# Kernel optimization log

Measured on AMD Instinct MI355X. Metric: run time of the kernel, lower is better.

Reference implementation:

```python
import jax, jax.numpy as jnp
import numpy as np

DIM = 1024

def setup_inputs() -> dict:
    key = jax.random.key(0)
    k1, k2, k3, k4 = jax.random.split(key, 4)
    scale = 1.0 / np.sqrt(DIM)
    return {
        "segment_embeds": jax.random.normal(k1, (32, 2048, DIM), dtype=jnp.float32),
        "Wq": jax.random.normal(k2, (DIM, DIM), dtype=jnp.float32) * scale,
        "bq": jax.random.normal(k3, (DIM,), dtype=jnp.float32) * scale,
        "mem_bank": jax.random.normal(k4, (131072, DIM), dtype=jnp.float32) * scale,
        "k": 8,
    }

def reference(segment_embeds, Wq, bq, mem_bank, k):
    # mean-pool over time: (B, C)
    segment_mean = segment_embeds.mean(axis=1)
    # linear query projection (torch Linear: x @ W.T + b)
    q = segment_mean @ Wq.T + bq
    # dense scores against memory bank: (B, M)
    attn_scores = (q @ mem_bank.T) / jnp.sqrt(jnp.asarray(DIM, dtype=q.dtype))
    # top-k select
    top_k_scores, top_k_indices = jax.lax.top_k(attn_scores, k)  # (B, K)
    attn_weights = jax.nn.softmax(top_k_scores, axis=-1)  # (B, K)
    # gather retrieved vectors: (B, K, C)
    retrieved_vectors = mem_bank[top_k_indices]
    # weighted sum over K, keepdim -> (B, 1, C)
    retrieved_mem = jnp.sum(attn_weights[..., None] * retrieved_vectors, axis=1, keepdims=True)
    return retrieved_mem
```

## Files before the change

### kernel.cpp

```cpp
#include <hip/hip_runtime.h>
#include <hip/hip_bf16.h>
#include <math.h>

#define NB 32
#define NT 2048
#define NC 1024
#define NM 131072
#define TOPK 8
#define NSB 256
#define ROWS_PB 512
#define NP 32
#define SLOTF 260
#define TILEF (4 * 16 * SLOTF)
#define SCOFF (2 * TILEF)
#define SMEMF (SCOFF + 2 * 32 * 17)

typedef __attribute__((ext_vector_type(8))) short s16x8;
typedef __attribute__((ext_vector_type(4))) float f32x4;
typedef __attribute__((ext_vector_type(4))) int i32x4;

#define OFF_PART 0
#define OFF_CS   0
#define OFF_CI   65536
#define OFF_MEAN 1048576
#define OFF_Q    (OFF_MEAN + 32768)
#define OFF_QB   (OFF_Q + 32768)

__device__ __forceinline__ unsigned short f2bf(float f) {
    unsigned u = __float_as_uint(f);
    unsigned r = (u + 0x7FFFu + ((u >> 16) & 1u)) >> 16;
    return (unsigned short)r;
}

__device__ __forceinline__ void gl_lds16(const float* g, float* l) {
    __builtin_amdgcn_global_load_lds((const __attribute__((address_space(1))) void*)g,
                                     (__attribute__((address_space(3))) void*)l, 16, 0, 0);
}

__global__ __launch_bounds__(256) void mean_partial_k(const float* __restrict__ seg,
                                                      float* __restrict__ part) {
    int blk = blockIdx.x;
    int b = blk >> 5, tc = blk & 31;
    int tid = threadIdx.x;
    const float4* src = (const float4*)(seg + ((size_t)b * NT + (size_t)tc * 64) * NC);
    float4 acc = make_float4(0.f, 0.f, 0.f, 0.f);
#pragma unroll 4
    for (int t = 0; t < 64; ++t) {
        float4 v = src[(size_t)t * 256 + tid];
        acc.x += v.x; acc.y += v.y; acc.z += v.z; acc.w += v.w;
    }
    ((float4*)(part + ((size_t)b * 32 + tc) * NC))[tid] = acc;
}

__global__ __launch_bounds__(256) void mean_finalize_k(const float* __restrict__ part,
                                                       float* __restrict__ mean) {
    int i = blockIdx.x * 256 + threadIdx.x;
    int b = i >> 10, c = i & 1023;
    float s = 0.f;
#pragma unroll
    for (int tc = 0; tc < 32; ++tc) s += part[((size_t)b * 32 + tc) * NC + c];
    mean[i] = s * (1.0f / NT);
}

__global__ __launch_bounds__(256) void qproj_k(const float* __restrict__ mean,
                                               const float* __restrict__ Wq,
                                               const float* __restrict__ bq,
                                               float* __restrict__ q) {
    int wave = (blockIdx.x * 256 + threadIdx.x) >> 6;
    int lane = threadIdx.x & 63;
    int o0 = wave * 16;
    for (int j = 0; j < 16; ++j) {
        int o = o0 + j;
        int b = o >> 10, i = o & 1023;
        const float4* wr = (const float4*)(Wq + (size_t)i * NC);
        const float4* mr = (const float4*)(mean + (size_t)b * NC);
        float acc = 0.f;
#pragma unroll
        for (int e = 0; e < 4; ++e) {
            float4 w4 = wr[lane * 4 + e];
            float4 m4 = mr[lane * 4 + e];
            acc += w4.x * m4.x + w4.y * m4.y + w4.z * m4.z + w4.w * m4.w;
        }
#pragma unroll
        for (int off = 32; off; off >>= 1) acc += __shfl_xor(acc, off);
        if (lane == 0) q[o] = acc + bq[i];
    }
}

__global__ __launch_bounds__(256) void qbf_k(const float* __restrict__ q,
                                             s16x8* __restrict__ qb) {
    int idx = blockIdx.x * 256 + threadIdx.x;
    int lane = idx & 63, n = (idx >> 6) & 1, ks = idx >> 7;
    int b = n * 16 + (lane & 15);
    int k0 = ks * 32 + ((lane >> 4) << 3);
    s16x8 v;
#pragma unroll
    for (int e = 0; e < 8; ++e) v[e] = (short)f2bf(q[(size_t)b * NC + k0 + e]);
    qb[idx] = v;
}

#define BUBBLE8(v, vi, s, si)                                   \
    {                                                           \
        float _v = (v); int _vi = (vi);                         \
        _Pragma("unroll")                                       \
        for (int _u = 0; _u < 8; ++_u) {                        \
            bool _gt = _v > s[_u];                               \
            float _ts = _gt ? _v : s[_u];                       \
            int _ti = _gt ? _vi : si[_u];                       \
            _v = _gt ? s[_u] : _v;                              \
            _vi = _gt ? si[_u] : _vi;                           \
            s[_u] = _ts; si[_u] = _ti;                          \
        }                                                       \
    }

#define BUBBLE8F(v, s)                                          \
    {                                                           \
        float _v = (v);                                         \
        _Pragma("unroll")                                       \
        for (int _u = 0; _u < 8; ++_u) {                        \
            bool _gt = _v > s[_u];                               \
            float _ts = _gt ? _v : s[_u];                       \
            _v = _gt ? s[_u] : _v;                              \
            s[_u] = _ts;                                        \
        }                                                       \
    }

__global__ __launch_bounds__(256, 1) void scores_mfma_k(const float* __restrict__ memb,
                                                        const s16x8* __restrict__ qb,
                                                        float* __restrict__ candS,
                                                        int* __restrict__ candI) {
    extern __shared__ __align__(16) float smemf[];
    int tid = threadIdx.x, lane = tid & 63, ws = tid >> 6;
    int n = ws & 1, kh = ws >> 1;
    size_t mb0 = (size_t)blockIdx.x * ROWS_PB;

    float s8[8];
#pragma unroll
    for (int u = 0; u < 8; ++u) s8[u] = -INFINITY;

#define TISSUE(p_) { float* lb = smemf + ((p_) & 1) * TILEF;                          \
    const float* gb = memb + (mb0 + (size_t)(p_) * 16) * NC + lane * 4;               \
    _Pragma("unroll") for (int i_ = 0; i_ < 16; ++i_) {                               \
        int r_ = ws * 4 + (i_ >> 2), c_ = i_ & 3;                                     \
        gl_lds16(gb + (size_t)r_ * NC + c_ * 256, lb + (c_ * 16 + r_) * SLOTF); } }

    s16x8 qf[16];
#pragma unroll
    for (int s = 0; s < 16; ++s)
        qf[s] = qb[((kh * 16 + s) * 2 + n) * 64 + lane];

    TISSUE(0);
    TISSUE(1);

    for (int p = 0; p < NP; ++p) {
        if (p + 1 < NP) { asm volatile("s_waitcnt vmcnt(16)" ::: "memory"); }
        else            { asm volatile("s_waitcnt vmcnt(0)" ::: "memory"); }
        __builtin_amdgcn_sched_barrier(0);
        __builtin_amdgcn_s_barrier();
        __builtin_amdgcn_sched_barrier(0);

        f32x4 acc = (f32x4){0.f, 0.f, 0.f, 0.f};
        const float* tb = smemf + (p & 1) * TILEF;
#pragma unroll
        for (int s = 0; s < 16; ++s) {
            int ksg = kh * 16 + s;
            const float* ap = tb + ((ksg >> 3) * 16 + (lane & 15)) * SLOTF
                            + (ksg & 7) * 32 + ((lane >> 4) << 3);
            uint4 lo = *(const uint4*)(ap);
            uint4 hi = *(const uint4*)(ap + 4);
            i32x4 ai;
            ai[0] = __builtin_amdgcn_perm(lo.y, lo.x, 0x07060302u);
            ai[1] = __builtin_amdgcn_perm(lo.w, lo.z, 0x07060302u);
            ai[2] = __builtin_amdgcn_perm(hi.y, hi.x, 0x07060302u);
            ai[3] = __builtin_amdgcn_perm(hi.w, hi.z, 0x07060302u);
            s16x8 a = __builtin_bit_cast(s16x8, ai);
            acc = __builtin_amdgcn_mfma_f32_16x16x32_bf16(a, qf[s], acc, 0, 0, 0);
        }

        {
            int bcol = n * 16 + (lane & 15);
            int mrow = (lane >> 4) << 2;
#pragma unroll
            for (int j = 0; j < 4; ++j)
                smemf[SCOFF + (kh * 32 + bcol) * 17 + mrow + j] = acc[j];
        }
        asm volatile("s_waitcnt lgkmcnt(0)" ::: "memory");
        __builtin_amdgcn_sched_barrier(0);
        __builtin_amdgcn_s_barrier();
        __builtin_amdgcn_sched_barrier(0);

        {
            int b = tid >> 3, pq = tid & 7;
#pragma unroll
            for (int rr = 0; rr < 2; ++rr) {
                int m = pq + rr * 8;
                float v = smemf[SCOFF + b * 17 + m]
                        + smemf[SCOFF + (32 + b) * 17 + m];
                unsigned uu = (__float_as_uint(v) & ~0x1FFu) | (unsigned)(p * 16 + m);
                BUBBLE8F(__uint_as_float(uu), s8);
            }
        }
        __builtin_amdgcn_sched_barrier(0);
        __builtin_amdgcn_s_barrier();
        __builtin_amdgcn_sched_barrier(0);

        if (p + 2 < NP) TISSUE(p + 2);
    }
#undef TISSUE

    {
        float* cs = smemf;
#pragma unroll
        for (int u = 0; u < 8; ++u) cs[tid * 9 + u] = s8[u];
        __syncthreads();
        float* csA = smemf + 2304;
        if (tid < 64) {
            float s2[8];
#pragma unroll
            for (int u = 0; u < 8; ++u) s2[u] = -INFINITY;
            int t0 = (tid >> 1) * 8 + (tid & 1) * 4;
            for (int tt = 0; tt < 4; ++tt)
#pragma unroll
                for (int u = 0; u < 8; ++u)
                    BUBBLE8F(cs[(t0 + tt) * 9 + u], s2);
#pragma unroll
            for (int u = 0; u < 8; ++u) csA[tid * 9 + u] = s2[u];
        }
        __syncthreads();
        if (tid < 32) {
            float s3[8];
#pragma unroll
            for (int u = 0; u < 8; ++u) s3[u] = -INFINITY;
            for (int j = 0; j < 16; ++j)
                BUBBLE8F(csA[(tid * 2 + (j >> 3)) * 9 + (j & 7)], s3);
#pragma unroll
            for (int u = 0; u < 8; ++u) {
                candS[((size_t)tid * NSB + blockIdx.x) * 8 + u] = s3[u] * 0.03125f;
                candI[((size_t)tid * NSB + blockIdx.x) * 8 + u] =
                    (int)mb0 + (int)(__float_as_uint(s3[u]) & 0x1FFu);
            }
        }
    }
}

__global__ __launch_bounds__(256) void finalize_k(const float* __restrict__ candS,
                                                  const int* __restrict__ candI,
                                                  const float* __restrict__ memb,
                                                  const float* __restrict__ q,
                                                  float* __restrict__ out) {
    __shared__ float cs[256 * 9];
    __shared__ int ci[256 * 9];
    __shared__ float csA[64 * 9];
    __shared__ int ciA[64 * 9];
    __shared__ float exsc[64];
    __shared__ int exid[64];
    __shared__ float wgt[8];
    __shared__ int widx[8];
    int b = blockIdx.x, tid = threadIdx.x;
    const float* S = candS + (size_t)b * (NSB * 8);
    const int* I = candI + (size_t)b * (NSB * 8);

    {
        float s[8]; int si[8];
#pragma unroll
        for (int u = 0; u < 8; ++u) { s[u] = -INFINITY; si[u] = -1; }
        for (int j = 0; j < 8; ++j)
            BUBBLE8(S[tid * 8 + j], I[tid * 8 + j], s, si);
#pragma unroll
        for (int u = 0; u < 8; ++u) { cs[tid * 9 + u] = s[u]; ci[tid * 9 + u] = si[u]; }
    }
    __syncthreads();
    if (tid < 64) {
        float s[8]; int si[8];
#pragma unroll
        for (int u = 0; u < 8; ++u) { s[u] = -INFINITY; si[u] = -1; }
        for (int tt = 0; tt < 4; ++tt)
#pragma unroll
            for (int u = 0; u < 8; ++u)
                BUBBLE8(cs[(tid * 4 + tt) * 9 + u], ci[(tid * 4 + tt) * 9 + u], s, si);
#pragma unroll
        for (int u = 0; u < 8; ++u) { csA[tid * 9 + u] = s[u]; ciA[tid * 9 + u] = si[u]; }
    }
    __syncthreads();
    if (tid < 8) {
        float s[8]; int si[8];
#pragma unroll
        for (int u = 0; u < 8; ++u) { s[u] = -INFINITY; si[u] = -1; }
        for (int tt = 0; tt < 8; ++tt)
#pragma unroll
            for (int u = 0; u < 8; ++u)
                BUBBLE8(csA[(tid * 8 + tt) * 9 + u], ciA[(tid * 8 + tt) * 9 + u], s, si);
#pragma unroll
        for (int u = 0; u < 8; ++u) exid[tid * 8 + u] = si[u];
    }
    __syncthreads();
    {
        int w = tid >> 6, lane = tid & 63;
        const float4* qr = (const float4*)(q + (size_t)b * NC);
        for (int i = 0; i < 16; ++i) {
            int c = w * 16 + i;
            int row = exid[c];
            const float4* mr = (const float4*)(memb + (size_t)row * NC);
            float d = 0.f;
#pragma unroll
            for (int e = 0; e < 4; ++e) {
                float4 m4 = mr[e * 64 + lane];
                float4 q4 = qr[e * 64 + lane];
                d += m4.x * q4.x + m4.y * q4.y + m4.z * q4.z + m4.w * q4.w;
            }
#pragma unroll
            for (int off = 32; off; off >>= 1) d += __shfl_xor(d, off);
            if (lane == 0) exsc[c] = d * 0.03125f;
        }
    }
    __syncthreads();
    if (tid == 0) {
        float s4[8]; int si4[8];
#pragma unroll
        for (int u = 0; u < 8; ++u) { s4[u] = -INFINITY; si4[u] = -1; }
        for (int j = 0; j < 64; ++j)
            BUBBLE8(exsc[j], exid[j], s4, si4);
        float m = s4[0], sum = 0.f, w[8];
#pragma unroll
        for (int u = 0; u < 8; ++u) { w[u] = __expf(s4[u] - m); sum += w[u]; }
        float inv = 1.0f / sum;
#pragma unroll
        for (int u = 0; u < 8; ++u) { wgt[u] = w[u] * inv; widx[u] = si4[u]; }
    }
    __syncthreads();
    {
        float wv[8]; int ix[8];
#pragma unroll
        for (int u = 0; u < 8; ++u) { wv[u] = wgt[u]; ix[u] = widx[u]; }
        float4 o = make_float4(0.f, 0.f, 0.f, 0.f);
#pragma unroll
        for (int u = 0; u < 8; ++u) {
            float4 r = ((const float4*)(memb + (size_t)ix[u] * NC))[tid];
            o.x = fmaf(wv[u], r.x, o.x);
            o.y = fmaf(wv[u], r.y, o.y);
            o.z = fmaf(wv[u], r.z, o.z);
            o.w = fmaf(wv[u], r.w, o.w);
        }
        ((float4*)(out + (size_t)b * NC))[tid] = o;
    }
}

extern "C" void kernel_launch(void* const* d_in, const int* in_sizes, int n_in,
                              void* d_out, int out_size, void* d_ws, size_t ws_size,
                              hipStream_t stream) {
    const float* seg  = (const float*)d_in[0];
    const float* Wq   = (const float*)d_in[1];
    const float* bq   = (const float*)d_in[2];
    const float* memb = (const float*)d_in[3];
    float* ws = (float*)d_ws;
    float* part  = ws + OFF_PART;
    float* mean  = ws + OFF_MEAN;
    float* q     = ws + OFF_Q;
    s16x8* qb    = (s16x8*)(ws + OFF_QB);
    float* candS = ws + OFF_CS;
    int*   candI = (int*)(ws + OFF_CI);
    float* out = (float*)d_out;

    (void)hipFuncSetAttribute((const void*)scores_mfma_k,
                              hipFuncAttributeMaxDynamicSharedMemorySize,
                              SMEMF * 4);

    mean_partial_k<<<NB * 32, 256, 0, stream>>>(seg, part);
    mean_finalize_k<<<(NB * NC) / 256, 256, 0, stream>>>(part, mean);
    qproj_k<<<512, 256, 0, stream>>>(mean, Wq, bq, q);
    qbf_k<<<16, 256, 0, stream>>>(q, qb);
    scores_mfma_k<<<NSB, 256, SMEMF * 4, stream>>>(memb, qb, candS, candI);
    finalize_k<<<NB, 256, 0, stream>>>(candS, candI, memb, q, out);
}
```

Baseline: 204.6 us.

## Double the score-kernel block to 512 threads and stage tiles through registers

Raises the scores kernel to 512 threads (8 waves), splitting the K dimension four ways so each wave runs 8 MFMAs per panel instead of 16. Tiles are now loaded through registers and written to LDS (register double-buffering) instead of the async global_load_lds path, and the per-panel top-k update uses one candidate per thread. The aim is more memory parallelism and latency hiding for streaming the memory bank, at the cost of an extra LDS write pass, more __syncthreads per panel, and a 4-way partial-sum reduction.

```diff
diff --git a/kernel.cpp b/kernel.cpp
--- a/kernel.cpp
+++ b/kernel.cpp
@@ -13,7 +13,7 @@
 #define SLOTF 260
 #define TILEF (4 * 16 * SLOTF)
 #define SCOFF (2 * TILEF)
-#define SMEMF (SCOFF + 2 * 32 * 17)
+#define SMEMF (SCOFF + 4 * 32 * 17)
 
 typedef __attribute__((ext_vector_type(8))) short s16x8;
 typedef __attribute__((ext_vector_type(4))) float f32x4;
@@ -30,11 +30,6 @@
     unsigned u = __float_as_uint(f);
     unsigned r = (u + 0x7FFFu + ((u >> 16) & 1u)) >> 16;
     return (unsigned short)r;
-}
-
-__device__ __forceinline__ void gl_lds16(const float* g, float* l) {
-    __builtin_amdgcn_global_load_lds((const __attribute__((address_space(1))) void*)g,
-                                     (__attribute__((address_space(3))) void*)l, 16, 0, 0);
 }
 
 __global__ __launch_bounds__(256) void mean_partial_k(const float* __restrict__ seg,
@@ -125,7 +120,7 @@
         }                                                       \
     }
 
-__global__ __launch_bounds__(256, 1) void scores_mfma_k(const float* __restrict__ memb,
+__global__ __launch_bounds__(512, 1) void scores_mfma_k(const float* __restrict__ memb,
                                                         const s16x8* __restrict__ qb,
                                                         float* __restrict__ candS,
                                                         int* __restrict__ candI) {
@@ -133,92 +128,92 @@
     int tid = threadIdx.x, lane = tid & 63, ws = tid >> 6;
     int n = ws & 1, kh = ws >> 1;
     size_t mb0 = (size_t)blockIdx.x * ROWS_PB;
+    const float4* gbase = (const float4*)(memb + mb0 * NC);
 
     float s8[8];
 #pragma unroll
     for (int u = 0; u < 8; ++u) s8[u] = -INFINITY;
 
-#define TISSUE(p_) { float* lb = smemf + ((p_) & 1) * TILEF;                          \
-    const float* gb = memb + (mb0 + (size_t)(p_) * 16) * NC + lane * 4;               \
-    _Pragma("unroll") for (int i_ = 0; i_ < 16; ++i_) {                               \
-        int r_ = ws * 4 + (i_ >> 2), c_ = i_ & 3;                                     \
-        gl_lds16(gb + (size_t)r_ * NC + c_ * 256, lb + (c_ * 16 + r_) * SLOTF); } }
-
-    s16x8 qf[16];
-#pragma unroll
-    for (int s = 0; s < 16; ++s)
-        qf[s] = qb[((kh * 16 + s) * 2 + n) * 64 + lane];
-
-    TISSUE(0);
-    TISSUE(1);
-
-    for (int p = 0; p < NP; ++p) {
-        if (p + 1 < NP) { asm volatile("s_waitcnt vmcnt(16)" ::: "memory"); }
-        else            { asm volatile("s_waitcnt vmcnt(0)" ::: "memory"); }
-        __builtin_amdgcn_sched_barrier(0);
-        __builtin_amdgcn_s_barrier();
-        __builtin_amdgcn_sched_barrier(0);
-
-        f32x4 acc = (f32x4){0.f, 0.f, 0.f, 0.f};
-        const float* tb = smemf + (p & 1) * TILEF;
-#pragma unroll
-        for (int s = 0; s < 16; ++s) {
-            int ksg = kh * 16 + s;
-            const float* ap = tb + ((ksg >> 3) * 16 + (lane & 15)) * SLOTF
-                            + (ksg & 7) * 32 + ((lane >> 4) << 3);
-            uint4 lo = *(const uint4*)(ap);
-            uint4 hi = *(const uint4*)(ap + 4);
-            i32x4 ai;
-            ai[0] = __builtin_amdgcn_perm(lo.y, lo.x, 0x07060302u);
-            ai[1] = __builtin_amdgcn_perm(lo.w, lo.z, 0x07060302u);
-            ai[2] = __builtin_amdgcn_perm(hi.y, hi.x, 0x07060302u);
-            ai[3] = __builtin_amdgcn_perm(hi.w, hi.z, 0x07060302u);
-            s16x8 a = __builtin_bit_cast(s16x8, ai);
-            acc = __builtin_amdgcn_mfma_f32_16x16x32_bf16(a, qf[s], acc, 0, 0, 0);
-        }
-
-        {
-            int bcol = n * 16 + (lane & 15);
-            int mrow = (lane >> 4) << 2;
-#pragma unroll
-            for (int j = 0; j < 4; ++j)
-                smemf[SCOFF + (kh * 32 + bcol) * 17 + mrow + j] = acc[j];
-        }
-        asm volatile("s_waitcnt lgkmcnt(0)" ::: "memory");
-        __builtin_amdgcn_sched_barrier(0);
-        __builtin_amdgcn_s_barrier();
-        __builtin_amdgcn_sched_barrier(0);
-
-        {
-            int b = tid >> 3, pq = tid & 7;
-#pragma unroll
-            for (int rr = 0; rr < 2; ++rr) {
-                int m = pq + rr * 8;
-                float v = smemf[SCOFF + b * 17 + m]
-                        + smemf[SCOFF + (32 + b) * 17 + m];
-                unsigned uu = (__float_as_uint(v) & ~0x1FFu) | (unsigned)(p * 16 + m);
-                BUBBLE8F(__uint_as_float(uu), s8);
-            }
-        }
-        __builtin_amdgcn_sched_barrier(0);
-        __builtin_amdgcn_s_barrier();
-        __builtin_amdgcn_sched_barrier(0);
-
-        if (p + 2 < NP) TISSUE(p + 2);
-    }
-#undef TISSUE
+    s16x8 qf[8];
+#pragma unroll
+    for (int s = 0; s < 8; ++s)
+        qf[s] = qb[(((kh * 8 + s) * 2) + n) * 64 + lane];
+
+    int lwoff[8];
+#pragma unroll
+    for (int i = 0; i < 8; ++i) {
+        int f = i * 512 + tid;
+        lwoff[i] = (((f >> 6) & 3) * 16 + (f >> 8)) * SLOTF + (f & 63) * 4;
+    }
+
+#define LOADR(dst_, p_) { const float4* gp = gbase + (size_t)(p_) * 4096;             \
+    _Pragma("unroll") for (int i_ = 0; i_ < 8; ++i_)                                  \
+        dst_[i_] = gp[i_ * 512 + tid];                                                \
+    __builtin_amdgcn_sched_barrier(0); }
+
+#define WRITEL(src_, buf_) { float* lb = smemf + (buf_) * TILEF;                      \
+    _Pragma("unroll") for (int i_ = 0; i_ < 8; ++i_)                                  \
+        *(float4*)(lb + lwoff[i_]) = src_[i_]; }
+
+#define DOPANEL(p_, rcur_, rnext_) {                                                  \
+    __syncthreads();                        \
+    WRITEL(rcur_, (p_) & 1);                                                          \
+    if ((p_) + 1 < NP) LOADR(rnext_, (p_) + 1);                                       \
+    __syncthreads();                                            \
+    f32x4 acc = (f32x4){0.f, 0.f, 0.f, 0.f};                                          \
+    const float* tb = smemf + ((p_) & 1) * TILEF;                                     \
+    _Pragma("unroll") for (int s = 0; s < 8; ++s) {                                   \
+        const float* ap = tb + (kh * 16 + (lane & 15)) * SLOTF                        \
+                        + s * 32 + ((lane >> 4) << 3);                                \
+        uint4 lo = *(const uint4*)(ap);                                               \
+        uint4 hi = *(const uint4*)(ap + 4);                                           \
+        i32x4 ai;                                                                     \
+        ai[0] = __builtin_amdgcn_perm(lo.y, lo.x, 0x07060302u);                       \
+        ai[1] = __builtin_amdgcn_perm(lo.w, lo.z, 0x07060302u);                       \
+        ai[2] = __builtin_amdgcn_perm(hi.y, hi.x, 0x07060302u);                       \
+        ai[3] = __builtin_amdgcn_perm(hi.w, hi.z, 0x07060302u);                       \
+        s16x8 a = __builtin_bit_cast(s16x8, ai);                                      \
+        acc = __builtin_amdgcn_mfma_f32_16x16x32_bf16(a, qf[s], acc, 0, 0, 0);        \
+    }                                                                                 \
+    {    \
+        int bcol = n * 16 + (lane & 15);                                              \
+        int mrow = (lane >> 4) << 2;                                                  \
+        _Pragma("unroll") for (int j = 0; j < 4; ++j)                                 \
+            smemf[SCOFF + (kh * 32 + bcol) * 17 + mrow + j] = acc[j];                 \
+    }                                                                                 \
+    __syncthreads();                                                  \
+    {      \
+        int b_ = tid >> 4, m_ = tid & 15;                                             \
+        float v = smemf[SCOFF + b_ * 17 + m_]                                         \
+                + smemf[SCOFF + (32 + b_) * 17 + m_]                                  \
+                + smemf[SCOFF + (64 + b_) * 17 + m_]                                  \
+                + smemf[SCOFF + (96 + b_) * 17 + m_];                                 \
+        unsigned uu = (__float_as_uint(v) & ~0x1FFu) | (unsigned)((p_) * 16 + m_);    \
+        BUBBLE8F(__uint_as_float(uu), s8);                                            \
+    } }
+
+    float4 rA[8], rB[8];
+    LOADR(rA, 0);
+    for (int p = 0; p < NP; p += 2) {
+        DOPANEL(p, rA, rB);
+        DOPANEL(p + 1, rB, rA);
+    }
+#undef LOADR
+#undef WRITEL
+#undef DOPANEL
 
     {
+        __syncthreads();
         float* cs = smemf;
 #pragma unroll
         for (int u = 0; u < 8; ++u) cs[tid * 9 + u] = s8[u];
         __syncthreads();
-        float* csA = smemf + 2304;
-        if (tid < 64) {
+        float* csA = smemf + 4608;
+        if (tid < 128) {
             float s2[8];
 #pragma unroll
             for (int u = 0; u < 8; ++u) s2[u] = -INFINITY;
-            int t0 = (tid >> 1) * 8 + (tid & 1) * 4;
+            int t0 = (tid >> 2) * 16 + (tid & 3) * 4;
             for (int tt = 0; tt < 4; ++tt)
 #pragma unroll
                 for (int u = 0; u < 8; ++u)
@@ -231,8 +226,8 @@
             float s3[8];
 #pragma unroll
             for (int u = 0; u < 8; ++u) s3[u] = -INFINITY;
-            for (int j = 0; j < 16; ++j)
-                BUBBLE8F(csA[(tid * 2 + (j >> 3)) * 9 + (j & 7)], s3);
+            for (int j = 0; j < 32; ++j)
+                BUBBLE8F(csA[(tid * 4 + (j >> 3)) * 9 + (j & 7)], s3);
 #pragma unroll
             for (int u = 0; u < 8; ++u) {
                 candS[((size_t)tid * NSB + blockIdx.x) * 8 + u] = s3[u] * 0.03125f;
@@ -369,6 +364,6 @@
     mean_finalize_k<<<(NB * NC) / 256, 256, 0, stream>>>(part, mean);
     qproj_k<<<512, 256, 0, stream>>>(mean, Wq, bq, q);
     qbf_k<<<16, 256, 0, stream>>>(q, qb);
-    scores_mfma_k<<<NSB, 256, SMEMF * 4, stream>>>(memb, qb, candS, candI);
+    scores_mfma_k<<<NSB, 512, SMEMF * 4, stream>>>(memb, qb, candS, candI);
     finalize_k<<<NB, 256, 0, stream>>>(candS, candI, memb, q, out);
 }
```

Result: slower. 385.1 us (+88.2%).

## Halve score-kernel tile to 256 rows and split K into two half panels

Applied to the files above, without the earlier changes.

The scores kernel now processes 256 memory-bank rows per block instead of 512, doubling the grid to 512 blocks. Each 16-row group is loaded in two half-K panels, which halves the LDS tile size and lets two blocks share a CU (launch bounds now 256,2). Accumulation carries across the two panels before the top-k update. The merge kernel is adjusted to read 16 candidates per thread to cover the larger candidate list. In exchange there are more barriers per row group and more candidates to merge.

```diff
diff --git a/kernel.cpp b/kernel.cpp
--- a/kernel.cpp
+++ b/kernel.cpp
@@ -7,11 +7,11 @@
 #define NC 1024
 #define NM 131072
 #define TOPK 8
-#define NSB 256
-#define ROWS_PB 512
-#define NP 32
+#define NSB 512
+#define ROWS_PB 256
+#define NPAN 32
 #define SLOTF 260
-#define TILEF (4 * 16 * SLOTF)
+#define TILEF (2 * 16 * SLOTF)
 #define SCOFF (2 * TILEF)
 #define SMEMF (SCOFF + 2 * 32 * 17)
 
@@ -21,7 +21,7 @@
 
 #define OFF_PART 0
 #define OFF_CS   0
-#define OFF_CI   65536
+#define OFF_CI   131072
 #define OFF_MEAN 1048576
 #define OFF_Q    (OFF_MEAN + 32768)
 #define OFF_QB   (OFF_Q + 32768)
@@ -125,7 +125,7 @@
         }                                                       \
     }
 
-__global__ __launch_bounds__(256, 1) void scores_mfma_k(const float* __restrict__ memb,
+__global__ __launch_bounds__(256, 2) void scores_mfma_k(const float* __restrict__ memb,
                                                         const s16x8* __restrict__ qb,
                                                         float* __restrict__ candS,
                                                         int* __restrict__ candI) {
@@ -138,34 +138,39 @@
 #pragma unroll
     for (int u = 0; u < 8; ++u) s8[u] = -INFINITY;
 
+    s16x8 qf[16];
+#pragma unroll
+    for (int g = 0; g < 2; ++g)
+#pragma unroll
+        for (int s = 0; s < 8; ++s)
+            qf[g * 8 + s] = qb[((g * 16 + kh * 8 + s) * 2 + n) * 64 + lane];
+    __builtin_amdgcn_sched_barrier(0);
+
 #define TISSUE(p_) { float* lb = smemf + ((p_) & 1) * TILEF;                          \
-    const float* gb = memb + (mb0 + (size_t)(p_) * 16) * NC + lane * 4;               \
-    _Pragma("unroll") for (int i_ = 0; i_ < 16; ++i_) {                               \
-        int r_ = ws * 4 + (i_ >> 2), c_ = i_ & 3;                                     \
+    const float* gb = memb + (mb0 + (size_t)((p_) >> 1) * 16) * NC                    \
+                    + ((p_) & 1) * 512 + lane * 4;                                    \
+    _Pragma("unroll") for (int i_ = 0; i_ < 8; ++i_) {                                \
+        int r_ = ws * 4 + (i_ >> 1), c_ = i_ & 1;                                     \
         gl_lds16(gb + (size_t)r_ * NC + c_ * 256, lb + (c_ * 16 + r_) * SLOTF); } }
-
-    s16x8 qf[16];
-#pragma unroll
-    for (int s = 0; s < 16; ++s)
-        qf[s] = qb[((kh * 16 + s) * 2 + n) * 64 + lane];
 
     TISSUE(0);
     TISSUE(1);
 
-    for (int p = 0; p < NP; ++p) {
-        if (p + 1 < NP) { asm volatile("s_waitcnt vmcnt(16)" ::: "memory"); }
-        else            { asm volatile("s_waitcnt vmcnt(0)" ::: "memory"); }
+    f32x4 acc = (f32x4){0.f, 0.f, 0.f, 0.f};
+    for (int p = 0; p < NPAN; ++p) {
+        int g = p & 1;
+        if (p + 1 < NPAN) { asm volatile("s_waitcnt vmcnt(8)" ::: "memory"); }
+        else              { asm volatile("s_waitcnt vmcnt(0)" ::: "memory"); }
         __builtin_amdgcn_sched_barrier(0);
         __builtin_amdgcn_s_barrier();
         __builtin_amdgcn_sched_barrier(0);
 
-        f32x4 acc = (f32x4){0.f, 0.f, 0.f, 0.f};
         const float* tb = smemf + (p & 1) * TILEF;
 #pragma unroll
-        for (int s = 0; s < 16; ++s) {
-            int ksg = kh * 16 + s;
-            const float* ap = tb + ((ksg >> 3) * 16 + (lane & 15)) * SLOTF
-                            + (ksg & 7) * 32 + ((lane >> 4) << 3);
+        for (int s = 0; s < 8; ++s) {
+            int l = kh * 8 + s;
+            const float* ap = tb + ((l >> 3) * 16 + (lane & 15)) * SLOTF
+                            + (l & 7) * 32 + ((lane >> 4) << 3);
             uint4 lo = *(const uint4*)(ap);
             uint4 hi = *(const uint4*)(ap + 4);
             i32x4 ai;
@@ -174,37 +179,39 @@
             ai[2] = __builtin_amdgcn_perm(hi.y, hi.x, 0x07060302u);
             ai[3] = __builtin_amdgcn_perm(hi.w, hi.z, 0x07060302u);
             s16x8 a = __builtin_bit_cast(s16x8, ai);
-            acc = __builtin_amdgcn_mfma_f32_16x16x32_bf16(a, qf[s], acc, 0, 0, 0);
-        }
-
-        {
-            int bcol = n * 16 + (lane & 15);
-            int mrow = (lane >> 4) << 2;
-#pragma unroll
-            for (int j = 0; j < 4; ++j)
-                smemf[SCOFF + (kh * 32 + bcol) * 17 + mrow + j] = acc[j];
-        }
-        asm volatile("s_waitcnt lgkmcnt(0)" ::: "memory");
+            acc = __builtin_amdgcn_mfma_f32_16x16x32_bf16(a, qf[g * 8 + s], acc, 0, 0, 0);
+        }
+
+        if (g == 1) {
+            int rg = p >> 1;
+            {
+                int bcol = n * 16 + (lane & 15);
+                int mrow = (lane >> 4) << 2;
+#pragma unroll
+                for (int j = 0; j < 4; ++j)
+                    smemf[SCOFF + (kh * 32 + bcol) * 17 + mrow + j] = acc[j];
+            }
+            asm volatile("s_waitcnt lgkmcnt(0)" ::: "memory");
+            __builtin_amdgcn_sched_barrier(0);
+            __builtin_amdgcn_s_barrier();
+            __builtin_amdgcn_sched_barrier(0);
+            {
+                int b = tid >> 3, pq = tid & 7;
+#pragma unroll
+                for (int rr = 0; rr < 2; ++rr) {
+                    int m = pq + rr * 8;
+                    float v = smemf[SCOFF + b * 17 + m]
+                            + smemf[SCOFF + (32 + b) * 17 + m];
+                    unsigned uu = (__float_as_uint(v) & ~0x1FFu) | (unsigned)(rg * 16 + m);
+                    BUBBLE8F(__uint_as_float(uu), s8);
+                }
+            }
+            acc = (f32x4){0.f, 0.f, 0.f, 0.f};
+        }
         __builtin_amdgcn_sched_barrier(0);
         __builtin_amdgcn_s_barrier();
         __builtin_amdgcn_sched_barrier(0);
-
-        {
-            int b = tid >> 3, pq = tid & 7;
-#pragma unroll
-            for (int rr = 0; rr < 2; ++rr) {
-                int m = pq + rr * 8;
-                float v = smemf[SCOFF + b * 17 + m]
-                        + smemf[SCOFF + (32 + b) * 17 + m];
-                unsigned uu = (__float_as_uint(v) & ~0x1FFu) | (unsigned)(p * 16 + m);
-                BUBBLE8F(__uint_as_float(uu), s8);
-            }
-        }
-        __builtin_amdgcn_sched_barrier(0);
-        __builtin_amdgcn_s_barrier();
-        __builtin_amdgcn_sched_barrier(0);
-
-        if (p + 2 < NP) TISSUE(p + 2);
+        if (p + 2 < NPAN) TISSUE(p + 2);
     }
 #undef TISSUE
 
@@ -264,8 +271,8 @@
         float s[8]; int si[8];
 #pragma unroll
         for (int u = 0; u < 8; ++u) { s[u] = -INFINITY; si[u] = -1; }
-        for (int j = 0; j < 8; ++j)
-            BUBBLE8(S[tid * 8 + j], I[tid * 8 + j], s, si);
+        for (int j = 0; j < 16; ++j)
+            BUBBLE8(S[tid * 16 + j], I[tid * 16 + j], s, si);
 #pragma unroll
         for (int u = 0; u < 8; ++u) { cs[tid * 9 + u] = s[u]; ci[tid * 9 + u] = si[u]; }
     }
```

After: 288.8 us. 41.1% more time.
